# Optimization experiments

Measured on AMD Instinct MI355X. Metric: run time of the kernel, lower is better.

Reference implementation:

```python
import jax, jax.numpy as jnp
import numpy as np

B = 32768

def _lin(x, w, b):
    return x @ w.T + b

def setup_inputs() -> dict:
    key = jax.random.key(0)
    ks = iter(jax.random.split(key, 40))
    def rn(shape, s=0.05):
        return jax.random.normal(next(ks), shape, dtype=jnp.float32) * s
    inp = {
        'img_feat': jax.random.normal(next(ks), (B, 256), dtype=jnp.float32),
        'instruction_idx': jax.random.randint(next(ks), (B, 1), 0, 4),
        '_hx': jax.random.normal(next(ks), (B, 256), dtype=jnp.float32),
        '_cx': jax.random.normal(next(ks), (B, 256), dtype=jnp.float32),
        'query': jax.random.normal(next(ks), (B, 256), dtype=jnp.float32),
        # parameters
        'emb': rn((4, 25), 1.0),
        'w_ta': rn((256, 25)), 'b_ta': rn((256,)),
        'w_ih': rn((1024, 512)), 'w_hh': rn((1024, 256)),
        'b_ih': rn((1024,)), 'b_hh': rn((1024,)),
        'w_q': rn((256, 256)), 'b_q': rn((256,)),
        'w_k': rn((256, 256)), 'b_k': rn((256,)),
        'w_ba': rn((512, 512)), 'b_ba': rn((512,)),
        'w_at': rn((256, 512)), 'b_at': rn((256,)),
        'w_p1': rn((128, 256)), 'b_p1': rn((128,)),
        'w_p2': rn((64, 128)), 'b_p2': rn((64,)),
        'w_p': rn((3, 64)), 'b_p': rn((3,)),
        'w_v1': rn((64, 256)), 'b_v1': rn((64,)),
        'w_v2': rn((32, 64)), 'b_v2': rn((32,)),
        'w_v': rn((1, 32)), 'b_v': rn((1,)),
    }
    return inp

def reference(img_feat, instruction_idx, _hx, _cx, query,
              emb, w_ta, b_ta, w_ih, w_hh, b_ih, b_hh,
              w_q, b_q, w_k, b_k, w_ba, b_ba, w_at, b_at,
              w_p1, b_p1, w_p2, b_p2, w_p, b_p,
              w_v1, b_v1, w_v2, b_v2, w_v, b_v):
    # embedding lookup [B,1,25] -> [B,25]
    we = emb[instruction_idx].reshape(instruction_idx.shape[0], -1)
    gated_att = jax.nn.sigmoid(_lin(we, w_ta, b_ta))          # [B,256]
    gated_fusion = img_feat * gated_att                        # [B,256]
    lstm_input = jnp.concatenate([gated_fusion, gated_att], 1) # [B,512]
    # LSTMCell (PyTorch gate order: i, f, g, o)
    gates = lstm_input @ w_ih.T + b_ih + _hx @ w_hh.T + b_hh   # [B,1024]
    i, f, g, o = jnp.split(gates, 4, axis=1)
    cx = jax.nn.sigmoid(f) * _cx + jax.nn.sigmoid(i) * jnp.tanh(g)
    hx = jax.nn.sigmoid(o) * jnp.tanh(cx)
    mlp_input = jnp.concatenate([gated_fusion, hx], 1)         # [B,512]
    mlp_attn = jax.nn.relu(_lin(mlp_input, w_ba, b_ba))        # [B,512]
    key_, val = jnp.split(mlp_attn, 2, axis=1)                 # [B,256] each
    w_q_out = jax.nn.relu(_lin(query, w_q, b_q))
    w_k_out = jax.nn.relu(_lin(key_, w_k, b_k))
    u_t = jnp.tanh(w_q_out + w_k_out)
    attention_vector = u_t * val
    attn_weight = jnp.concatenate([attention_vector, hx], 1)   # [B,512]
    attn_weight = jax.nn.relu(_lin(attn_weight, w_at, b_at))   # [B,256]
    pol = jax.nn.relu(_lin(attn_weight, w_p1, b_p1))
    pol = jax.nn.relu(_lin(pol, w_p2, b_p2))
    valh = jax.nn.relu(_lin(attn_weight, w_v1, b_v1))
    valh = jax.nn.relu(_lin(valh, w_v2, b_v2))
    return (_lin(valh, w_v, b_v), _lin(pol, w_p, b_p), hx, cx)
```

## Files before the change

### kernel.cpp

```cpp
#include <hip/hip_runtime.h>

typedef unsigned short u16;
typedef __bf16 bf16x8 __attribute__((ext_vector_type(8)));
typedef float f32x4 __attribute__((ext_vector_type(4)));
typedef u16 u16x8 __attribute__((ext_vector_type(8)));
typedef u16 u16x4 __attribute__((ext_vector_type(4)));

#define TM 64
#define LDP 264
#define BTOT 32768

#define OFF_WIH 0
#define OFF_WHH 524288
#define OFF_WQ  786432
#define OFF_WK  851968
#define OFF_WBA 917504
#define OFF_WAT 1179648
#define OFF_WP1 1310720
#define OFF_WP2 1343488
#define OFF_WV1 1351680
#define OFF_WV2 1368064
#define OFF_G   1370112

__device__ __forceinline__ float b2f(u16 h) {
    union { unsigned int u; float f; } v; v.u = ((unsigned int)h) << 16; return v.f;
}
__device__ __forceinline__ u16 f2b(float f) {
    union { float f; unsigned int u; } v; v.f = f;
    unsigned int u = v.u + 0x7fffu + ((v.u >> 16) & 1u);
    return (u16)(u >> 16);
}
__device__ __forceinline__ float sigm(float x) { return 1.0f / (1.0f + __expf(-x)); }
__device__ __forceinline__ float tanhfast(float x) { return 1.0f - 2.0f / (__expf(2.0f * x) + 1.0f); }
__device__ __forceinline__ float relu(float x) { return x > 0.0f ? x : 0.0f; }
__device__ __forceinline__ bf16x8 ld8(const u16* p) { return *(const bf16x8*)p; }
__device__ __forceinline__ f32x4 mfma16(bf16x8 a, bf16x8 b, f32x4 c) {
    return __builtin_amdgcn_mfma_f32_16x16x32_bf16(a, b, c, 0, 0, 0);
}

__device__ __forceinline__ bool detect_f32(const void* imgp) {
    const unsigned int* w = (const unsigned int*)imgp;
    int hits = 0;
    #pragma unroll
    for (int i = 0; i < 16; ++i) {
        int e0 = (w[i] >> 7) & 0xFF;
        hits += (e0 >= 100 && e0 <= 140) ? 1 : 0;
    }
    return hits < 10;
}

__device__ __forceinline__ float ldin(const void* p, size_t i, bool f32) {
    return f32 ? ((const float*)p)[i] : b2f(((const u16*)p)[i]);
}
__device__ __forceinline__ void stout_nt(void* o, size_t i, float v, bool f32) {
    if (f32) __builtin_nontemporal_store(v, (float*)o + i);
    else ((u16*)o)[i] = f2b(v);
}
__device__ __forceinline__ f32x4 ld4(const void* p, size_t i, bool f32) {
    if (f32) return __builtin_nontemporal_load((const f32x4*)((const float*)p + i));
    u16x4 q = *(const u16x4*)((const u16*)p + i);
    f32x4 r;
    #pragma unroll
    for (int j = 0; j < 4; ++j) r[j] = b2f(q[j]);
    return r;
}
__device__ __forceinline__ void st4(void* o, size_t i, f32x4 v, bool f32) {
    if (f32) __builtin_nontemporal_store(v, (f32x4*)((float*)o + i));
    else {
        u16x4 p;
        #pragma unroll
        for (int j = 0; j < 4; ++j) p[j] = f2b(v[j]);
        *(u16x4*)((u16*)o + i) = p;
    }
}
__device__ __forceinline__ bf16x8 ldg8f_nt(const void* p, size_t i, bool f32) {
    u16 t[8];
    if (f32) {
        const f32x4* q = (const f32x4*)((const float*)p + i);
        f32x4 a = __builtin_nontemporal_load(q);
        f32x4 b = __builtin_nontemporal_load(q + 1);
        #pragma unroll
        for (int j = 0; j < 4; ++j) { t[j] = f2b(a[j]); t[4 + j] = f2b(b[j]); }
    } else {
        *(u16x8*)t = *(const u16x8*)((const u16*)p + i);
    }
    return *(bf16x8*)t;
}

struct CvtArgs {
    const void* src[10];
    unsigned int nchunk[10];
    unsigned int off8[10];
    unsigned int Kdim[10];
    const void* emb;
    const void* w_ta;
    const void* b_ta;
    const void* det;
};

__global__ __launch_bounds__(256) void cvt_weights(CvtArgs a, u16* ws) {
    const bool f32 = detect_f32(a.det);
    const int p = blockIdx.x;
    if (p == 10) {
        if (blockIdx.y == 0) {
            for (int j = threadIdx.x; j < 1024; j += 256) {
                int e = j >> 8, n = j & 255;
                float acc = ldin(a.b_ta, n, f32);
                #pragma unroll
                for (int k = 0; k < 25; ++k)
                    acc += ldin(a.emb, e * 25 + k, f32) * ldin(a.w_ta, n * 25 + k, f32);
                ws[OFF_G + j] = f2b(sigm(acc));
            }
        }
        return;
    }
    const void* s = a.src[p];
    const unsigned int K = a.Kdim[p];
    const unsigned int sh = 31 - __clz((int)(K >> 5));
    const unsigned int cpr = K >> 3;
    const unsigned int csh = sh + 2;
    const unsigned int n = a.nchunk[p];
    for (unsigned int e = blockIdx.y * blockDim.x + threadIdx.x; e < n;
         e += gridDim.y * blockDim.x) {
        const unsigned int row  = e >> csh;
        const unsigned int colc = e & (cpr - 1u);
        const unsigned int g = ((((row >> 4) << sh) + (colc >> 2)) << 6)
                             + ((colc & 3u) << 4) + (row & 15u);
        const size_t si = ((size_t)e) << 3;
        u16 t[8];
        if (f32) {
            const f32x4* q = (const f32x4*)((const float*)s + si);
            f32x4 va = *q;
            f32x4 vb = *(q + 1);
            #pragma unroll
            for (int j = 0; j < 4; ++j) { t[j] = f2b(va[j]); t[4 + j] = f2b(vb[j]); }
        } else {
            *(u16x8*)t = *(const u16x8*)((const u16*)s + si);
        }
        ((u16x8*)ws)[a.off8[p] + g] = *(u16x8*)t;
    }
}

__global__ __launch_bounds__(1024, 2) void ac_fused(
    const void* __restrict__ img, const int* __restrict__ insn,
    const void* __restrict__ hx_in, const void* __restrict__ cx_in,
    const void* __restrict__ query,
    const void* __restrict__ b_ih, const void* __restrict__ b_hh,
    const void* __restrict__ b_q, const void* __restrict__ b_k,
    const void* __restrict__ b_ba, const void* __restrict__ b_at,
    const void* __restrict__ b_p1, const void* __restrict__ b_p2,
    const void* __restrict__ w_p3, const void* __restrict__ b_p3,
    const void* __restrict__ b_v1, const void* __restrict__ b_v2,
    const void* __restrict__ w_v3, const void* __restrict__ b_v3,
    const u16* __restrict__ wsb, void* __restrict__ out)
{
    __shared__ __align__(16) u16 sGF[TM * LDP];
    __shared__ __align__(16) u16 sHX0[TM * LDP];
    __shared__ __align__(16) u16 sHX1[TM * LDP];
    __shared__ __align__(16) u16 sKEY[TM * LDP];
    __shared__ __align__(16) u16 sG[4 * LDP];
    __shared__ int sIDX[TM];

    const bool isf32 = detect_f32(img);
    const int tid  = threadIdx.x;
    const int lane = tid & 63;
    const int wv   = tid >> 6;
    const int l15  = lane & 15;
    const int quad = lane >> 4;
    const int q8   = quad * 8;
    const int q4   = quad * 4;
    const int ln8  = lane * 8;
    const int row0 = blockIdx.x * TM;

    const int r0s = tid >> 5, c0s = (tid & 31) << 3;
    const int r1s = (tid + 1024) >> 5;
    float iv0[8], hv0[8], iv1[8], hv1[8];
    {
        const size_t base0 = (size_t)(row0 + r0s) * 256 + c0s;
        const size_t base1 = (size_t)(row0 + r1s) * 256 + c0s;
        if (isf32) {
            const f32x4* ip0 = (const f32x4*)((const float*)img + base0);
            const f32x4* hp0 = (const f32x4*)((const float*)hx_in + base0);
            const f32x4* ip1 = (const f32x4*)((const float*)img + base1);
            const f32x4* hp1 = (const f32x4*)((const float*)hx_in + base1);
            f32x4 a0 = __builtin_nontemporal_load(ip0);
            f32x4 a1 = __builtin_nontemporal_load(ip0 + 1);
            f32x4 b0 = __builtin_nontemporal_load(hp0);
            f32x4 b1 = __builtin_nontemporal_load(hp0 + 1);
            f32x4 c0 = __builtin_nontemporal_load(ip1);
            f32x4 c1 = __builtin_nontemporal_load(ip1 + 1);
            f32x4 d0 = __builtin_nontemporal_load(hp1);
            f32x4 d1 = __builtin_nontemporal_load(hp1 + 1);
            #pragma unroll
            for (int j = 0; j < 4; ++j) {
                iv0[j] = a0[j]; iv0[4 + j] = a1[j];
                hv0[j] = b0[j]; hv0[4 + j] = b1[j];
                iv1[j] = c0[j]; iv1[4 + j] = c1[j];
                hv1[j] = d0[j]; hv1[4 + j] = d1[j];
            }
        } else {
            u16x8 i80 = *(const u16x8*)((const u16*)img + base0);
            u16x8 h80 = *(const u16x8*)((const u16*)hx_in + base0);
            u16x8 i81 = *(const u16x8*)((const u16*)img + base1);
            u16x8 h81 = *(const u16x8*)((const u16*)hx_in + base1);
            #pragma unroll
            for (int j = 0; j < 8; ++j) {
                iv0[j] = b2f(i80[j]); hv0[j] = b2f(h80[j]);
                iv1[j] = b2f(i81[j]); hv1[j] = b2f(h81[j]);
            }
        }
    }
    if (tid < TM) sIDX[tid] = insn[row0 + tid];
    sG[(tid >> 8) * LDP + (tid & 255)] = wsb[OFF_G + tid];
    __syncthreads();

    {
        int e0 = sIDX[r0s], e1 = sIDX[r1s];
        u16x8 gv0 = *(const u16x8*)(sG + e0 * LDP + c0s);
        u16x8 gv1 = *(const u16x8*)(sG + e1 * LDP + c0s);
        u16x8 ov0, hvv0, ov1, hvv1;
        #pragma unroll
        for (int j = 0; j < 8; ++j) {
            ov0[j] = f2b(iv0[j] * b2f(gv0[j]));  hvv0[j] = f2b(hv0[j]);
            ov1[j] = f2b(iv1[j] * b2f(gv1[j]));  hvv1[j] = f2b(hv1[j]);
        }
        *(u16x8*)(sGF + r0s * LDP + c0s) = ov0;
        *(u16x8*)(sHX0 + r0s * LDP + c0s) = hvv0;
        *(u16x8*)(sGF + r1s * LDP + c0s) = ov1;
        *(u16x8*)(sHX0 + r1s * LDP + c0s) = hvv1;
    }
    __syncthreads();

    {
        int eIdx[4];
        #pragma unroll
        for (int m = 0; m < 4; ++m) eIdx[m] = sIDX[m * 16 + l15];
        const u16* bih0 = wsb + OFF_WIH + ln8;
        const u16* bhh0 = wsb + OFF_WHH + ln8;
        const int c = wv;
        f32x4 acc[4][4] = {};
        #pragma unroll
        for (int kk = 0; kk < 8; ++kk) {
            bf16x8 a[4], b[4];
            #pragma unroll
            for (int m = 0; m < 4; ++m) a[m] = ld8(sGF + (m * 16 + l15) * LDP + kk * 32 + q8);
            #pragma unroll
            for (int g = 0; g < 4; ++g) b[g] = ld8(bih0 + (size_t)((g * 16 + c) * 16 + kk) * 512);
            #pragma unroll
            for (int g = 0; g < 4; ++g)
                #pragma unroll
                for (int m = 0; m < 4; ++m) acc[g][m] = mfma16(b[g], a[m], acc[g][m]);
        }
        #pragma unroll
        for (int kk = 0; kk < 8; ++kk) {
            bf16x8 a[4], b[4];
            #pragma unroll
            for (int m = 0; m < 4; ++m) a[m] = ld8(sG + eIdx[m] * LDP + kk * 32 + q8);
            #pragma unroll
            for (int g = 0; g < 4; ++g) b[g] = ld8(bih0 + (size_t)((g * 16 + c) * 16 + 8 + kk) * 512);
            #pragma unroll
            for (int g = 0; g < 4; ++g)
                #pragma unroll
                for (int m = 0; m < 4; ++m) acc[g][m] = mfma16(b[g], a[m], acc[g][m]);
        }
        #pragma unroll
        for (int kk = 0; kk < 8; ++kk) {
            bf16x8 a[4], b[4];
            #pragma unroll
            for (int m = 0; m < 4; ++m) a[m] = ld8(sHX0 + (m * 16 + l15) * LDP + kk * 32 + q8);
            #pragma unroll
            for (int g = 0; g < 4; ++g) b[g] = ld8(bhh0 + (size_t)((g * 16 + c) * 8 + kk) * 512);
            #pragma unroll
            for (int g = 0; g < 4; ++g)
                #pragma unroll
                for (int m = 0; m < 4; ++m) acc[g][m] = mfma16(b[g], a[m], acc[g][m]);
        }
        const int nbase = c * 16 + q4;
        float bI[4], bF[4], bG[4], bO[4];
        #pragma unroll
        for (int r = 0; r < 4; ++r) {
            bI[r] = ldin(b_ih,       nbase + r, isf32) + ldin(b_hh,       nbase + r, isf32);
            bF[r] = ldin(b_ih, 256 + nbase + r, isf32) + ldin(b_hh, 256 + nbase + r, isf32);
            bG[r] = ldin(b_ih, 512 + nbase + r, isf32) + ldin(b_hh, 512 + nbase + r, isf32);
            bO[r] = ldin(b_ih, 768 + nbase + r, isf32) + ldin(b_hh, 768 + nbase + r, isf32);
        }
        #pragma unroll
        for (int m = 0; m < 4; ++m) {
            const int batch = m * 16 + l15;
            const size_t gbase = (size_t)(row0 + batch) * 256 + nbase;
            f32x4 cxo = ld4(cx_in, gbase, isf32);
            f32x4 hnv, cnv; u16x4 hpk;
            #pragma unroll
            for (int r = 0; r < 4; ++r) {
                const float iv = sigm(acc[0][m][r] + bI[r]);
                const float fv = sigm(acc[1][m][r] + bF[r]);
                const float gv = tanhfast(acc[2][m][r] + bG[r]);
                const float ov = sigm(acc[3][m][r] + bO[r]);
                const float cn = fv * cxo[r] + iv * gv;
                const float hn = ov * tanhfast(cn);
                cnv[r] = cn; hnv[r] = hn; hpk[r] = f2b(hn);
            }
            st4(out, (size_t)(4 * BTOT) + gbase, hnv, isf32);
            st4(out, (size_t)(4 * BTOT) + (size_t)256 * BTOT + gbase, cnv, isf32);
            *(u16x4*)(sHX1 + batch * LDP + nbase) = hpk;
        }
    }
    __syncthreads();

    {
        f32x4 acc[2][4] = {};
        const u16* bb0 = wsb + OFF_WBA + ln8;
        #pragma unroll
        for (int kk = 0; kk < 8; ++kk) {
            bf16x8 a[4], b[2];
            #pragma unroll
            for (int m = 0; m < 4; ++m) a[m] = ld8(sGF + (m * 16 + l15) * LDP + kk * 32 + q8);
            #pragma unroll
            for (int t = 0; t < 2; ++t) b[t] = ld8(bb0 + (size_t)((wv * 2 + t) * 16 + kk) * 512);
            #pragma unroll
            for (int t = 0; t < 2; ++t)
                #pragma unroll
                for (int m = 0; m < 4; ++m) acc[t][m] = mfma16(b[t], a[m], acc[t][m]);
        }
        #pragma unroll
        for (int kk = 0; kk < 8; ++kk) {
            bf16x8 a[4], b[2];
            #pragma unroll
            for (int m = 0; m < 4; ++m) a[m] = ld8(sHX1 + (m * 16 + l15) * LDP + kk * 32 + q8);
            #pragma unroll
            for (int t = 0; t < 2; ++t) b[t] = ld8(bb0 + (size_t)((wv * 2 + t) * 16 + 8 + kk) * 512);
            #pragma unroll
            for (int t = 0; t < 2; ++t)
                #pragma unroll
                for (int m = 0; m < 4; ++m) acc[t][m] = mfma16(b[t], a[m], acc[t][m]);
        }
        #pragma unroll
        for (int t = 0; t < 2; ++t) {
            const int colb = (wv * 2 + t) * 16 + q4;
            float bb[4];
            #pragma unroll
            for (int r = 0; r < 4; ++r) bb[r] = ldin(b_ba, colb + r, isf32);
            u16* dst = (colb < 256) ? (sKEY + colb) : (sHX0 + (colb - 256));
            #pragma unroll
            for (int m = 0; m < 4; ++m) {
                u16x4 pk;
                #pragma unroll
                for (int r = 0; r < 4; ++r) pk[r] = f2b(relu(acc[t][m][r] + bb[r]));
                *(u16x4*)(dst + (m * 16 + l15) * LDP) = pk;
            }
        }
    }
    __syncthreads();

    {
        f32x4 cq[4] = {}, ck[4] = {};
        const u16* bq0 = wsb + OFF_WQ + ln8;
        const u16* bk0 = wsb + OFF_WK + ln8;
        #pragma unroll
        for (int kk = 0; kk < 8; ++kk) {
            bf16x8 aq[4], ak[4], bqf, bkf;
            #pragma unroll
            for (int m = 0; m < 4; ++m) {
                aq[m] = ldg8f_nt(query, (size_t)(row0 + m * 16 + l15) * 256 + kk * 32 + q8, isf32);
                ak[m] = ld8(sKEY + (m * 16 + l15) * LDP + kk * 32 + q8);
            }
            bqf = ld8(bq0 + (size_t)(wv * 8 + kk) * 512);
            bkf = ld8(bk0 + (size_t)(wv * 8 + kk) * 512);
            #pragma unroll
            for (int m = 0; m < 4; ++m) {
                cq[m] = mfma16(bqf, aq[m], cq[m]);
                ck[m] = mfma16(bkf, ak[m], ck[m]);
            }
        }
        const int nbase = wv * 16 + q4;
        float bqv[4], bkv[4];
        #pragma unroll
        for (int r = 0; r < 4; ++r) {
            bqv[r] = ldin(b_q, nbase + r, isf32);
            bkv[r] = ldin(b_k, nbase + r, isf32);
        }
        #pragma unroll
        for (int m = 0; m < 4; ++m) {
            const int batch = m * 16 + l15;
            u16x4 vv = *(const u16x4*)(sHX0 + batch * LDP + nbase);
            u16x4 pk;
            #pragma unroll
            for (int r = 0; r < 4; ++r) {
                const float u = tanhfast(relu(cq[m][r] + bqv[r]) + relu(ck[m][r] + bkv[r]));
                pk[r] = f2b(u * b2f(vv[r]));
            }
            *(u16x4*)(sGF + batch * LDP + nbase) = pk;
        }
    }
    __syncthreads();

    {
        f32x4 acc[4] = {};
        const u16* bb0 = wsb + OFF_WAT + ln8;
        #pragma unroll
        for (int kk = 0; kk < 8; ++kk) {
            bf16x8 a[4], b;
            #pragma unroll
            for (int m = 0; m < 4; ++m) a[m] = ld8(sGF + (m * 16 + l15) * LDP + kk * 32 + q8);
            b = ld8(bb0 + (size_t)(wv * 16 + kk) * 512);
            #pragma unroll
            for (int m = 0; m < 4; ++m) acc[m] = mfma16(b, a[m], acc[m]);
        }
        #pragma unroll
        for (int kk = 0; kk < 8; ++kk) {
            bf16x8 a[4], b;
            #pragma unroll
            for (int m = 0; m < 4; ++m) a[m] = ld8(sHX1 + (m * 16 + l15) * LDP + kk * 32 + q8);
            b = ld8(bb0 + (size_t)(wv * 16 + 8 + kk) * 512);
            #pragma unroll
            for (int m = 0; m < 4; ++m) acc[m] = mfma16(b, a[m], acc[m]);
        }
        const int nbase = wv * 16 + q4;
        float bb[4];
        #pragma unroll
        for (int r = 0; r < 4; ++r) bb[r] = ldin(b_at, nbase + r, isf32);
        #pragma unroll
        for (int m = 0; m < 4; ++m) {
            u16x4 pk;
            #pragma unroll
            for (int r = 0; r < 4; ++r) pk[r] = f2b(relu(acc[m][r] + bb[r]));
            *(u16x4*)(sKEY + (m * 16 + l15) * LDP + nbase) = pk;
        }
    }
    __syncthreads();

    {
        const int m = wv & 3, half = wv >> 2;
        const int batch = m * 16 + l15;
        bf16x8 afr[8];
        #pragma unroll
        for (int kk = 0; kk < 8; ++kk) afr[kk] = ld8(sKEY + batch * LDP + kk * 32 + q8);
        {
            f32x4 acc[2] = {};
            #pragma unroll
            for (int kk = 0; kk < 8; ++kk)
                #pragma unroll
                for (int t = 0; t < 2; ++t)
                    acc[t] = mfma16(ld8(wsb + OFF_WP1 + (size_t)((half * 2 + t) * 8 + kk) * 512 + ln8), afr[kk], acc[t]);
            #pragma unroll
            for (int t = 0; t < 2; ++t) {
                const int colb = (half * 2 + t) * 16 + q4;
                u16x4 pk;
                #pragma unroll
                for (int r = 0; r < 4; ++r) pk[r] = f2b(relu(acc[t][r] + ldin(b_p1, colb + r, isf32)));
                *(u16x4*)(sHX0 + batch * LDP + colb) = pk;
            }
        }
        {
            f32x4 acc = {};
            #pragma unroll
            for (int kk = 0; kk < 8; ++kk)
                acc = mfma16(ld8(wsb + OFF_WV1 + (size_t)(half * 8 + kk) * 512 + ln8), afr[kk], acc);
            const int colb = half * 16 + q4;
            u16x4 pk;
            #pragma unroll
            for (int r = 0; r < 4; ++r) pk[r] = f2b(relu(acc[r] + ldin(b_v1, colb + r, isf32)));
            *(u16x4*)(sHX0 + batch * LDP + 128 + colb) = pk;
        }
    }
    __syncthreads();

    {
        const int m = wv & 3, half = wv >> 2;
        const int batch = m * 16 + l15;
        const u16* a0 = sHX0 + batch * LDP;
        bf16x8 ap[4], av2[2];
        #pragma unroll
        for (int kk = 0; kk < 4; ++kk) ap[kk] = ld8(a0 + kk * 32 + q8);
        #pragma unroll
        for (int kk = 0; kk < 2; ++kk) av2[kk] = ld8(a0 + 128 + kk * 32 + q8);
        {
            f32x4 acc = {};
            #pragma unroll
            for (int kk = 0; kk < 4; ++kk)
                acc = mfma16(ld8(wsb + OFF_WP2 + (size_t)(half * 4 + kk) * 512 + ln8), ap[kk], acc);
            const int colb = half * 16 + q4;
            u16x4 pk;
            #pragma unroll
            for (int r = 0; r < 4; ++r) pk[r] = f2b(relu(acc[r] + ldin(b_p2, colb + r, isf32)));
            *(u16x4*)(sGF + batch * LDP + colb) = pk;
        }
        if (half < 2) {
            f32x4 acc = {};
            #pragma unroll
            for (int kk = 0; kk < 2; ++kk)
                acc = mfma16(ld8(wsb + OFF_WV2 + (size_t)(half * 2 + kk) * 512 + ln8), av2[kk], acc);
            const int colb = half * 16 + q4;
            u16x4 pk;
            #pragma unroll
            for (int r = 0; r < 4; ++r) pk[r] = f2b(relu(acc[r] + ldin(b_v2, colb + r, isf32)));
            *(u16x4*)(sGF + batch * LDP + 64 + colb) = pk;
        }
    }
    __syncthreads();

    if (tid < TM * 4) {
        const int r = tid >> 2, o = tid & 3;
        const int grow = row0 + r;
        const u16* rowp = sGF + r * LDP;
        if (o < 3) {
            float acc = ldin(b_p3, o, isf32);
            #pragma unroll
            for (int k = 0; k < 64; ++k) acc += b2f(rowp[k]) * ldin(w_p3, o * 64 + k, isf32);
            stout_nt(out, (size_t)BTOT + (size_t)grow * 3 + o, acc, isf32);
        } else {
            float acc = ldin(b_v3, 0, isf32);
            #pragma unroll
            for (int k = 0; k < 32; ++k) acc += b2f(rowp[64 + k]) * ldin(w_v3, k, isf32);
            stout_nt(out, (size_t)grow, acc, isf32);
        }
    }
}

extern "C" void kernel_launch(void* const* d_in, const int* in_sizes, int n_in,
                              void* d_out, int out_size, void* d_ws, size_t ws_size,
                              hipStream_t stream) {
    u16* ws = (u16*)d_ws;

    CvtArgs ca;
    const int srcIdx[10] = {8, 9, 12, 14, 16, 18, 20, 22, 26, 28};
    const unsigned int ns[10]   = {524288, 262144, 65536, 65536, 262144, 131072, 32768, 8192, 16384, 2048};
    const unsigned int off[10]  = {OFF_WIH, OFF_WHH, OFF_WQ, OFF_WK, OFF_WBA, OFF_WAT, OFF_WP1, OFF_WP2, OFF_WV1, OFF_WV2};
    const unsigned int kd[10]   = {512, 256, 256, 256, 512, 512, 256, 128, 256, 64};
    for (int i = 0; i < 10; ++i) {
        ca.src[i] = d_in[srcIdx[i]];
        ca.nchunk[i] = ns[i] / 8;
        ca.off8[i] = off[i] / 8;
        ca.Kdim[i] = kd[i];
    }
    ca.emb = d_in[5];
    ca.w_ta = d_in[6];
    ca.b_ta = d_in[7];
    ca.det = d_in[0];
    cvt_weights<<<dim3(11, 64), dim3(256), 0, stream>>>(ca, ws);

    ac_fused<<<dim3(BTOT / TM), dim3(1024), 0, stream>>>(
        d_in[0], (const int*)d_in[1], d_in[2], d_in[3], d_in[4],
        d_in[10], d_in[11],
        d_in[13], d_in[15],
        d_in[17], d_in[19],
        d_in[21], d_in[23],
        d_in[24], d_in[25],
        d_in[27], d_in[29],
        d_in[30], d_in[31],
        (const u16*)d_ws, d_out);
}
```

Measured before the change: 405.8 us.

## Reschedule independent GEMMs across barriers and fold biases into accumulator init

Moves the query projection GEMM (which does not depend on earlier stages) into the stage before the key/value MLP. It also starts the hx half of the w_at GEMM before the attention stage, so work is spread more evenly between barriers and the global query load overlaps other work. Biases are now loaded as vectors and used as the MFMA accumulator's starting value instead of being added per element in the epilogues. The small final-layer weights are staged into shared memory. The cost is more live accumulators carried across barriers, which raises register pressure at 1024 threads per block.

```diff
diff --git a/kernel.cpp b/kernel.cpp
--- a/kernel.cpp
+++ b/kernel.cpp
@@ -58,6 +58,14 @@
 }
 __device__ __forceinline__ f32x4 ld4(const void* p, size_t i, bool f32) {
     if (f32) return __builtin_nontemporal_load((const f32x4*)((const float*)p + i));
+    u16x4 q = *(const u16x4*)((const u16*)p + i);
+    f32x4 r;
+    #pragma unroll
+    for (int j = 0; j < 4; ++j) r[j] = b2f(q[j]);
+    return r;
+}
+__device__ __forceinline__ f32x4 ld4p(const void* p, size_t i, bool f32) {
+    if (f32) return *(const f32x4*)((const float*)p + i);
     u16x4 q = *(const u16x4*)((const u16*)p + i);
     f32x4 r;
     #pragma unroll
@@ -159,6 +167,7 @@
     __shared__ __align__(16) u16 sHX1[TM * LDP];
     __shared__ __align__(16) u16 sKEY[TM * LDP];
     __shared__ __align__(16) u16 sG[4 * LDP];
+    __shared__ float sW3[224];
     __shared__ int sIDX[TM];
 
     const bool isf32 = detect_f32(img);
@@ -171,6 +180,7 @@
     const int q4   = quad * 4;
     const int ln8  = lane * 8;
     const int row0 = blockIdx.x * TM;
+    const int nb16 = wv * 16 + q4;
 
     const int r0s = tid >> 5, c0s = (tid & 31) << 3;
     const int r1s = (tid + 1024) >> 5;
@@ -238,7 +248,14 @@
         const u16* bih0 = wsb + OFF_WIH + ln8;
         const u16* bhh0 = wsb + OFF_WHH + ln8;
         const int c = wv;
-        f32x4 acc[4][4] = {};
+        f32x4 acc[4][4];
+        #pragma unroll
+        for (int g = 0; g < 4; ++g) {
+            f32x4 bs = ld4p(b_ih, g * 256 + nb16, isf32)
+                     + ld4p(b_hh, g * 256 + nb16, isf32);
+            #pragma unroll
+            for (int m = 0; m < 4; ++m) acc[g][m] = bs;
+        }
         #pragma unroll
         for (int kk = 0; kk < 8; ++kk) {
             bf16x8 a[4], b[4];
@@ -274,42 +291,56 @@
             for (int g = 0; g < 4; ++g)
                 #pragma unroll
                 for (int m = 0; m < 4; ++m) acc[g][m] = mfma16(b[g], a[m], acc[g][m]);
-        }
-        const int nbase = c * 16 + q4;
-        float bI[4], bF[4], bG[4], bO[4];
-        #pragma unroll
-        for (int r = 0; r < 4; ++r) {
-            bI[r] = ldin(b_ih,       nbase + r, isf32) + ldin(b_hh,       nbase + r, isf32);
-            bF[r] = ldin(b_ih, 256 + nbase + r, isf32) + ldin(b_hh, 256 + nbase + r, isf32);
-            bG[r] = ldin(b_ih, 512 + nbase + r, isf32) + ldin(b_hh, 512 + nbase + r, isf32);
-            bO[r] = ldin(b_ih, 768 + nbase + r, isf32) + ldin(b_hh, 768 + nbase + r, isf32);
         }
         #pragma unroll
         for (int m = 0; m < 4; ++m) {
             const int batch = m * 16 + l15;
-            const size_t gbase = (size_t)(row0 + batch) * 256 + nbase;
+            const size_t gbase = (size_t)(row0 + batch) * 256 + nb16;
             f32x4 cxo = ld4(cx_in, gbase, isf32);
             f32x4 hnv, cnv; u16x4 hpk;
             #pragma unroll
             for (int r = 0; r < 4; ++r) {
-                const float iv = sigm(acc[0][m][r] + bI[r]);
-                const float fv = sigm(acc[1][m][r] + bF[r]);
-                const float gv = tanhfast(acc[2][m][r] + bG[r]);
-                const float ov = sigm(acc[3][m][r] + bO[r]);
+                const float iv = sigm(acc[0][m][r]);
+                const float fv = sigm(acc[1][m][r]);
+                const float gv = tanhfast(acc[2][m][r]);
+                const float ov = sigm(acc[3][m][r]);
                 const float cn = fv * cxo[r] + iv * gv;
                 const float hn = ov * tanhfast(cn);
                 cnv[r] = cn; hnv[r] = hn; hpk[r] = f2b(hn);
             }
             st4(out, (size_t)(4 * BTOT) + gbase, hnv, isf32);
             st4(out, (size_t)(4 * BTOT) + (size_t)256 * BTOT + gbase, cnv, isf32);
-            *(u16x4*)(sHX1 + batch * LDP + nbase) = hpk;
-        }
-    }
-    __syncthreads();
-
-    {
-        f32x4 acc[2][4] = {};
+            *(u16x4*)(sHX1 + batch * LDP + nb16) = hpk;
+        }
+    }
+    __syncthreads();
+
+    f32x4 cq[4];
+    {
+        {
+            f32x4 bq4 = ld4p(b_q, nb16, isf32);
+            #pragma unroll
+            for (int m = 0; m < 4; ++m) cq[m] = bq4;
+        }
+        const u16* bq0 = wsb + OFF_WQ + ln8;
+        #pragma unroll
+        for (int kk = 0; kk < 8; ++kk) {
+            bf16x8 aq[4];
+            #pragma unroll
+            for (int m = 0; m < 4; ++m)
+                aq[m] = ldg8f_nt(query, (size_t)(row0 + m * 16 + l15) * 256 + kk * 32 + q8, isf32);
+            bf16x8 bqf = ld8(bq0 + (size_t)(wv * 8 + kk) * 512);
+            #pragma unroll
+            for (int m = 0; m < 4; ++m) cq[m] = mfma16(bqf, aq[m], cq[m]);
+        }
         const u16* bb0 = wsb + OFF_WBA + ln8;
+        f32x4 acc[2][4];
+        #pragma unroll
+        for (int t = 0; t < 2; ++t) {
+            f32x4 bb4 = ld4p(b_ba, (wv * 2 + t) * 16 + q4, isf32);
+            #pragma unroll
+            for (int m = 0; m < 4; ++m) acc[t][m] = bb4;
+        }
         #pragma unroll
         for (int kk = 0; kk < 8; ++kk) {
             bf16x8 a[4], b[2];
@@ -337,106 +368,100 @@
         #pragma unroll
         for (int t = 0; t < 2; ++t) {
             const int colb = (wv * 2 + t) * 16 + q4;
-            float bb[4];
-            #pragma unroll
-            for (int r = 0; r < 4; ++r) bb[r] = ldin(b_ba, colb + r, isf32);
             u16* dst = (colb < 256) ? (sKEY + colb) : (sHX0 + (colb - 256));
             #pragma unroll
             for (int m = 0; m < 4; ++m) {
                 u16x4 pk;
                 #pragma unroll
-                for (int r = 0; r < 4; ++r) pk[r] = f2b(relu(acc[t][m][r] + bb[r]));
+                for (int r = 0; r < 4; ++r) pk[r] = f2b(relu(acc[t][m][r]));
                 *(u16x4*)(dst + (m * 16 + l15) * LDP) = pk;
             }
         }
     }
     __syncthreads();
 
-    {
-        f32x4 cq[4] = {}, ck[4] = {};
-        const u16* bq0 = wsb + OFF_WQ + ln8;
+    f32x4 acc4[4];
+    {
+        const u16* bat0 = wsb + OFF_WAT + ln8;
+        {
+            f32x4 bat4 = ld4p(b_at, nb16, isf32);
+            #pragma unroll
+            for (int m = 0; m < 4; ++m) acc4[m] = bat4;
+        }
+        #pragma unroll
+        for (int kk = 0; kk < 8; ++kk) {
+            bf16x8 a[4];
+            #pragma unroll
+            for (int m = 0; m < 4; ++m) a[m] = ld8(sHX1 + (m * 16 + l15) * LDP + kk * 32 + q8);
+            bf16x8 b = ld8(bat0 + (size_t)(wv * 16 + 8 + kk) * 512);
+            #pragma unroll
+            for (int m = 0; m < 4; ++m) acc4[m] = mfma16(b, a[m], acc4[m]);
+        }
+        f32x4 ck[4];
+        {
+            f32x4 bk4 = ld4p(b_k, nb16, isf32);
+            #pragma unroll
+            for (int m = 0; m < 4; ++m) ck[m] = bk4;
+        }
         const u16* bk0 = wsb + OFF_WK + ln8;
         #pragma unroll
         for (int kk = 0; kk < 8; ++kk) {
-            bf16x8 aq[4], ak[4], bqf, bkf;
-            #pragma unroll
-            for (int m = 0; m < 4; ++m) {
-                aq[m] = ldg8f_nt(query, (size_t)(row0 + m * 16 + l15) * 256 + kk * 32 + q8, isf32);
-                ak[m] = ld8(sKEY + (m * 16 + l15) * LDP + kk * 32 + q8);
-            }
-            bqf = ld8(bq0 + (size_t)(wv * 8 + kk) * 512);
-            bkf = ld8(bk0 + (size_t)(wv * 8 + kk) * 512);
-            #pragma unroll
-            for (int m = 0; m < 4; ++m) {
-                cq[m] = mfma16(bqf, aq[m], cq[m]);
-                ck[m] = mfma16(bkf, ak[m], ck[m]);
-            }
-        }
-        const int nbase = wv * 16 + q4;
-        float bqv[4], bkv[4];
-        #pragma unroll
-        for (int r = 0; r < 4; ++r) {
-            bqv[r] = ldin(b_q, nbase + r, isf32);
-            bkv[r] = ldin(b_k, nbase + r, isf32);
+            bf16x8 ak[4];
+            #pragma unroll
+            for (int m = 0; m < 4; ++m) ak[m] = ld8(sKEY + (m * 16 + l15) * LDP + kk * 32 + q8);
+            bf16x8 bkf = ld8(bk0 + (size_t)(wv * 8 + kk) * 512);
+            #pragma unroll
+            for (int m = 0; m < 4; ++m) ck[m] = mfma16(bkf, ak[m], ck[m]);
         }
         #pragma unroll
         for (int m = 0; m < 4; ++m) {
             const int batch = m * 16 + l15;
-            u16x4 vv = *(const u16x4*)(sHX0 + batch * LDP + nbase);
+            u16x4 vv = *(const u16x4*)(sHX0 + batch * LDP + nb16);
             u16x4 pk;
             #pragma unroll
             for (int r = 0; r < 4; ++r) {
-                const float u = tanhfast(relu(cq[m][r] + bqv[r]) + relu(ck[m][r] + bkv[r]));
+                const float u = tanhfast(relu(cq[m][r]) + relu(ck[m][r]));
                 pk[r] = f2b(u * b2f(vv[r]));
             }
-            *(u16x4*)(sGF + batch * LDP + nbase) = pk;
-        }
-    }
-    __syncthreads();
-
-    {
-        f32x4 acc[4] = {};
-        const u16* bb0 = wsb + OFF_WAT + ln8;
-        #pragma unroll
-        for (int kk = 0; kk < 8; ++kk) {
-            bf16x8 a[4], b;
+            *(u16x4*)(sGF + batch * LDP + nb16) = pk;
+        }
+    }
+    __syncthreads();
+
+    {
+        const u16* bat0 = wsb + OFF_WAT + ln8;
+        #pragma unroll
+        for (int kk = 0; kk < 8; ++kk) {
+            bf16x8 a[4];
             #pragma unroll
             for (int m = 0; m < 4; ++m) a[m] = ld8(sGF + (m * 16 + l15) * LDP + kk * 32 + q8);
-            b = ld8(bb0 + (size_t)(wv * 16 + kk) * 512);
-            #pragma unroll
-            for (int m = 0; m < 4; ++m) acc[m] = mfma16(b, a[m], acc[m]);
-        }
-        #pragma unroll
-        for (int kk = 0; kk < 8; ++kk) {
-            bf16x8 a[4], b;
-            #pragma unroll
-            for (int m = 0; m < 4; ++m) a[m] = ld8(sHX1 + (m * 16 + l15) * LDP + kk * 32 + q8);
-            b = ld8(bb0 + (size_t)(wv * 16 + 8 + kk) * 512);
-            #pragma unroll
-            for (int m = 0; m < 4; ++m) acc[m] = mfma16(b, a[m], acc[m]);
-        }
-        const int nbase = wv * 16 + q4;
-        float bb[4];
-        #pragma unroll
-        for (int r = 0; r < 4; ++r) bb[r] = ldin(b_at, nbase + r, isf32);
+            bf16x8 b = ld8(bat0 + (size_t)(wv * 16 + kk) * 512);
+            #pragma unroll
+            for (int m = 0; m < 4; ++m) acc4[m] = mfma16(b, a[m], acc4[m]);
+        }
         #pragma unroll
         for (int m = 0; m < 4; ++m) {
             u16x4 pk;
             #pragma unroll
-            for (int r = 0; r < 4; ++r) pk[r] = f2b(relu(acc[m][r] + bb[r]));
-            *(u16x4*)(sKEY + (m * 16 + l15) * LDP + nbase) = pk;
-        }
-    }
-    __syncthreads();
-
-    {
+            for (int r = 0; r < 4; ++r) pk[r] = f2b(relu(acc4[m][r]));
+            *(u16x4*)(sKEY + (m * 16 + l15) * LDP + nb16) = pk;
+        }
+    }
+    __syncthreads();
+
+    {
+        if (tid < 224)
+            sW3[tid] = (tid < 192) ? ldin(w_p3, tid, isf32)
+                                   : ldin(w_v3, tid - 192, isf32);
         const int m = wv & 3, half = wv >> 2;
         const int batch = m * 16 + l15;
         bf16x8 afr[8];
         #pragma unroll
         for (int kk = 0; kk < 8; ++kk) afr[kk] = ld8(sKEY + batch * LDP + kk * 32 + q8);
         {
-            f32x4 acc[2] = {};
+            f32x4 acc[2];
+            #pragma unroll
+            for (int t = 0; t < 2; ++t) acc[t] = ld4p(b_p1, (half * 2 + t) * 16 + q4, isf32);
             #pragma unroll
             for (int kk = 0; kk < 8; ++kk)
                 #pragma unroll
@@ -447,19 +472,19 @@
                 const int colb = (half * 2 + t) * 16 + q4;
                 u16x4 pk;
                 #pragma unroll
-                for (int r = 0; r < 4; ++r) pk[r] = f2b(relu(acc[t][r] + ldin(b_p1, colb + r, isf32)));
+                for (int r = 0; r < 4; ++r) pk[r] = f2b(relu(acc[t][r]));
                 *(u16x4*)(sHX0 + batch * LDP + colb) = pk;
             }
         }
         {
-            f32x4 acc = {};
+            f32x4 acc = ld4p(b_v1, half * 16 + q4, isf32);
             #pragma unroll
             for (int kk = 0; kk < 8; ++kk)
                 acc = mfma16(ld8(wsb + OFF_WV1 + (size_t)(half * 8 + kk) * 512 + ln8), afr[kk], acc);
             const int colb = half * 16 + q4;
             u16x4 pk;
             #pragma unroll
-            for (int r = 0; r < 4; ++r) pk[r] = f2b(relu(acc[r] + ldin(b_v1, colb + r, isf32)));
+            for (int r = 0; r < 4; ++r) pk[r] = f2b(relu(acc[r]));
             *(u16x4*)(sHX0 + batch * LDP + 128 + colb) = pk;
         }
     }
@@ -475,25 +500,25 @@
         #pragma unroll
         for (int kk = 0; kk < 2; ++kk) av2[kk] = ld8(a0 + 128 + kk * 32 + q8);
         {
-            f32x4 acc = {};
+            f32x4 acc = ld4p(b_p2, half * 16 + q4, isf32);
             #pragma unroll
             for (int kk = 0; kk < 4; ++kk)
                 acc = mfma16(ld8(wsb + OFF_WP2 + (size_t)(half * 4 + kk) * 512 + ln8), ap[kk], acc);
             const int colb = half * 16 + q4;
             u16x4 pk;
             #pragma unroll
-            for (int r = 0; r < 4; ++r) pk[r] = f2b(relu(acc[r] + ldin(b_p2, colb + r, isf32)));
+            for (int r = 0; r < 4; ++r) pk[r] = f2b(relu(acc[r]));
             *(u16x4*)(sGF + batch * LDP + colb) = pk;
         }
         if (half < 2) {
-            f32x4 acc = {};
+            f32x4 acc = ld4p(b_v2, half * 16 + q4, isf32);
             #pragma unroll
             for (int kk = 0; kk < 2; ++kk)
                 acc = mfma16(ld8(wsb + OFF_WV2 + (size_t)(half * 2 + kk) * 512 + ln8), av2[kk], acc);
             const int colb = half * 16 + q4;
             u16x4 pk;
             #pragma unroll
-            for (int r = 0; r < 4; ++r) pk[r] = f2b(relu(acc[r] + ldin(b_v2, colb + r, isf32)));
+            for (int r = 0; r < 4; ++r) pk[r] = f2b(relu(acc[r]));
             *(u16x4*)(sGF + batch * LDP + 64 + colb) = pk;
         }
     }
@@ -506,12 +531,12 @@
         if (o < 3) {
             float acc = ldin(b_p3, o, isf32);
             #pragma unroll
-            for (int k = 0; k < 64; ++k) acc += b2f(rowp[k]) * ldin(w_p3, o * 64 + k, isf32);
+            for (int k = 0; k < 64; ++k) acc += b2f(rowp[k]) * sW3[o * 64 + k];
             stout_nt(out, (size_t)BTOT + (size_t)grow * 3 + o, acc, isf32);
         } else {
             float acc = ldin(b_v3, 0, isf32);
             #pragma unroll
-            for (int k = 0; k < 32; ++k) acc += b2f(rowp[64 + k]) * ldin(w_v3, k, isf32);
+            for (int k = 0; k < 32; ++k) acc += b2f(rowp[64 + k]) * sW3[192 + k];
             stout_nt(out, (size_t)grow, acc, isf32);
         }
     }
```

Result: no change. 409.6 us (+0.9%).
